# Performance work log

Hardware: AMD Instinct MI355X
Metric: run time of the kernel (lower is better)

Reference implementation:

```python
import jax, jax.numpy as jnp
import numpy as np

HID = 7168; H = 128; DQ = 1536; DKV = 512; DH = 128; DR = 64; MAXS = 4096

def _rope_tables(seq_len):
    inv_freq = 1.0 / (10000.0 ** (jnp.arange(0, DR, 2, dtype=jnp.float32) / DR))
    t = jnp.arange(seq_len, dtype=jnp.float32)
    freqs = jnp.outer(t, inv_freq)              # [S, DR/2]
    emb = jnp.concatenate([freqs, freqs], -1)   # [S, DR]
    return jnp.cos(emb), jnp.sin(emb)

def _apply_rope(x, cos, sin):
    # x: [..., S, DR]; cos/sin: [S, DR]
    d = x.shape[-1]
    x1, x2 = x[..., : d // 2], x[..., d // 2 :]
    rotated = jnp.concatenate([-x2, x1], -1)
    return (x * cos + rotated * sin).astype(x.dtype)

def setup_inputs() -> dict:
    key = jax.random.key(0)
    ks = jax.random.split(key, 16)
    s = 0.02
    inp = {
        "h":    jax.random.normal(ks[0], (1, 1024, HID), jnp.float32),
        "Wdq":  jax.random.normal(ks[1], (DQ, HID), jnp.float32) * s,
        "bdq":  jnp.zeros((DQ,), jnp.float32),
        "Wdkv": jax.random.normal(ks[2], (DKV, HID), jnp.float32) * s,
        "bdkv": jnp.zeros((DKV,), jnp.float32),
        "Wuq":  jax.random.normal(ks[3], (H * DH, DQ), jnp.float32) * s,
        "buq":  jnp.zeros((H * DH,), jnp.float32),
        "Wukv": jax.random.normal(ks[4], (H * DH * 2, DKV), jnp.float32) * s,
        "bukv": jnp.zeros((H * DH * 2,), jnp.float32),
        "Wrq":  jax.random.normal(ks[5], (H * DR, DQ), jnp.float32) * s,
        "brq":  jnp.zeros((H * DR,), jnp.float32),
        "Wrk":  jax.random.normal(ks[6], (DR, HID), jnp.float32) * s,
        "brk":  jnp.zeros((DR,), jnp.float32),
        "Wo":   jax.random.normal(ks[7], (HID, H * DH), jnp.float32) * s,
        "bo":   jnp.zeros((HID,), jnp.float32),
    }
    return inp

def reference(h, Wdq, bdq, Wdkv, bdkv, Wuq, buq, Wukv, bukv, Wrq, brq, Wrk, brk, Wo, bo):
    B, S, _ = h.shape
    c_q = h @ Wdq.T + bdq              # [B,S,DQ]
    c_kv = h @ Wdkv.T + bdkv           # [B,S,DKV]
    q_c = (c_q @ Wuq.T + buq).reshape(B, S, H, DH).transpose(0, 2, 1, 3)     # [B,H,S,DH]
    kv_c = (c_kv @ Wukv.T + bukv).reshape(B, S, H, 2 * DH).transpose(0, 2, 1, 3)
    k_c, v = kv_c[..., :DH], kv_c[..., DH:]                                  # [B,H,S,DH]
    q_r = (c_q @ Wrq.T + brq).reshape(B, S, H, DR).transpose(0, 2, 1, 3)     # [B,H,S,DR]
    k_r = (h @ Wrk.T + brk).reshape(B, S, 1, DR).transpose(0, 2, 1, 3)       # [B,1,S,DR]
    cos, sin = _rope_tables(S)
    q_r = _apply_rope(q_r, cos, sin)
    k_r = _apply_rope(k_r, cos, sin)
    q = jnp.concatenate([q_c, q_r], -1)                                      # [B,H,S,DH+DR]
    k = jnp.concatenate([k_c, jnp.broadcast_to(k_r, (B, H, S, DR))], -1)
    scale = 1.0 / jnp.sqrt(jnp.float32(DH + DR))
    scores = jnp.einsum('bhqd,bhkd->bhqk', q, k) * scale
    attn = jax.nn.softmax(scores, axis=-1)
    o = jnp.einsum('bhqk,bhkd->bhqd', attn, v)        # [B,H,S,DH]
    o = o.transpose(0, 2, 1, 3).reshape(B, S, H * DH)
    return o @ Wo.T + bo
```

## Files before the change

### kernel.cpp

```cpp
#include <hip/hip_runtime.h>
#include <hip/hip_bf16.h>

#define S_LEN 1024
#define HID 7168
#define NH 128
#define DQ 1536
#define DKV 512
#define DH 128
#define DR 64

typedef __attribute__((ext_vector_type(8))) short bf16x8;
typedef __attribute__((ext_vector_type(4))) float f32x4;
typedef __attribute__((ext_vector_type(4))) float fl4;
typedef __attribute__((ext_vector_type(4))) unsigned short us4;
typedef __attribute__((ext_vector_type(8))) unsigned short us8;
typedef __attribute__((ext_vector_type(4))) unsigned int u32x4;

static __device__ __forceinline__ unsigned short f2bf(float f) {
  union { float f; unsigned int u; } v; v.f = f;
  unsigned int u = v.u;
  return (unsigned short)((u + 0x7fffu + ((u >> 16) & 1u)) >> 16);
}
static __device__ __forceinline__ float bf2f(unsigned short u) {
  union { unsigned int u; float f; } v; v.u = ((unsigned int)u) << 16;
  return v.f;
}
static __device__ __forceinline__ unsigned int cvtpk2(float lo, float hi) {
  unsigned int r;
  asm("v_cvt_pk_bf16_f32 %0, %1, %2" : "=v"(r) : "v"(lo), "v"(hi));
  return r;
}

__global__ __launch_bounds__(256) void cvt_bf16_kernel(
    const float* __restrict__ in, unsigned short* __restrict__ out, int n8) {
  int i = blockIdx.x * 256 + threadIdx.x;
  int stride = gridDim.x * 256;
  for (; i < n8; i += stride) {
    fl4 a = ((const fl4*)in)[2 * i];
    fl4 b = ((const fl4*)in)[2 * i + 1];
    us8 u = { f2bf(a[0]), f2bf(a[1]), f2bf(a[2]), f2bf(a[3]),
              f2bf(b[0]), f2bf(b[1]), f2bf(b[2]), f2bf(b[3]) };
    ((us8*)out)[i] = u;
  }
}

template <int OUTMODE, int WFP32, int ROPEQ = 0>
__global__ __launch_bounds__(256) void gemm_k(
    const unsigned short* __restrict__ A, int lda,
    const unsigned short* __restrict__ Wb16,
    const float* __restrict__ Wfa, const float* __restrict__ Wfb, int nsplit,
    int ldw,
    const float* __restrict__ bias,
    void* __restrict__ Cv, int ldc, size_t zstride,
    int Ncl, int ksl, float alpha,
    const float* __restrict__ ctab = nullptr,
    const float* __restrict__ stab = nullptr)
{
  const int n0 = blockIdx.x * 128;
  if (n0 >= Ncl) return;

  __shared__ unsigned short As[128 * 64];
  __shared__ unsigned short Ws[128 * 64];
  const int t = threadIdx.x;
  const int l = t & 63, w = t >> 6;
  const int r15 = l & 15, g = l >> 4;
  const int wm = (w >> 1) * 64, wn = (w & 1) * 64;
  const int m0 = blockIdx.y * 128;
  const int kbase = blockIdx.z * ksl;
  const int srow = l >> 3;
  const int scol = (l & 7) * 8;

  f32x4 acc[4][4];
#pragma unroll
  for (int i = 0; i < 4; ++i)
#pragma unroll
    for (int j = 0; j < 4; ++j) acc[i][j] = (f32x4){0.f, 0.f, 0.f, 0.f};

  const unsigned short* Ab = A + (size_t)m0 * lda;
  const unsigned short* Wb = nullptr;
  const float* Wf = nullptr;
  if constexpr (WFP32) {
    Wf = (n0 < nsplit) ? Wfa + (size_t)n0 * ldw : Wfb + (size_t)(n0 - nsplit) * ldw;
  } else {
    Wb = Wb16 + (size_t)n0 * ldw;
  }

  fl4 wx[4], wy[4];
  auto issueW = [&](int k0) {
#pragma unroll
    for (int i = 0; i < 4; ++i) {
      int c = t + 256 * i;
      const float* src = Wf + (size_t)(c >> 3) * ldw + k0 + (c & 7) * 8;
      wx[i] = *(const fl4*)src;
      wy[i] = *(const fl4*)(src + 4);
    }
  };

  if constexpr (WFP32) issueW(kbase);
  const int kend = kbase + ksl;

  for (int k0 = kbase; k0 < kend; k0 += 64) {
    __syncthreads();
#pragma unroll
    for (int i = 0; i < 4; ++i) {
      int chunk = w * 4 + i;
      int row = chunk * 8 + srow;
      __builtin_amdgcn_global_load_lds(
          (const __attribute__((address_space(1))) void*)(Ab + (size_t)row * lda + k0 + scol),
          (__attribute__((address_space(3))) void*)(As + chunk * 512), 16, 0, 0);
      if constexpr (!WFP32) {
        __builtin_amdgcn_global_load_lds(
            (const __attribute__((address_space(1))) void*)(Wb + (size_t)row * ldw + k0 + scol),
            (__attribute__((address_space(3))) void*)(Ws + chunk * 512), 16, 0, 0);
      }
    }
    if constexpr (WFP32) {
#pragma unroll
      for (int i = 0; i < 4; ++i) {
        int c = t + 256 * i;
        u32x4 p = { cvtpk2(wx[i][0], wx[i][1]), cvtpk2(wx[i][2], wx[i][3]),
                    cvtpk2(wy[i][0], wy[i][1]), cvtpk2(wy[i][2], wy[i][3]) };
        ((u32x4*)Ws)[c] = p;
      }
    }
    __syncthreads();
    if constexpr (WFP32) {
      if (k0 + 64 < kend) issueW(k0 + 64);
    }
#pragma unroll
    for (int kk = 0; kk < 2; ++kk) {
      bf16x8 a[4], b[4];
#pragma unroll
      for (int mt = 0; mt < 4; ++mt)
        a[mt] = *reinterpret_cast<const bf16x8*>(&As[(wm + mt * 16 + r15) * 64 + kk * 32 + 8 * g]);
#pragma unroll
      for (int nt = 0; nt < 4; ++nt)
        b[nt] = *reinterpret_cast<const bf16x8*>(&Ws[(wn + nt * 16 + r15) * 64 + kk * 32 + 8 * g]);
#pragma unroll
      for (int mt = 0; mt < 4; ++mt)
#pragma unroll
        for (int nt = 0; nt < 4; ++nt)
          acc[mt][nt] = __builtin_amdgcn_mfma_f32_16x16x32_bf16(a[mt], b[nt], acc[mt][nt], 0, 0, 0);
    }
  }

  if constexpr (OUTMODE == 1) {
    float bv[4];
#pragma unroll
    for (int nt = 0; nt < 4; ++nt) {
      int col = n0 + wn + nt * 16 + r15;
      bv[nt] = (col < Ncl) ? bias[col] : 0.f;
    }
    bool isrope = false;
    if constexpr (ROPEQ) isrope = (n0 + wn) >= 16384;
    if (ROPEQ && isrope) {
#pragma unroll
      for (int mt = 0; mt < 4; ++mt)
#pragma unroll
        for (int r = 0; r < 4; ++r) {
          int row = m0 + wm + mt * 16 + g * 4 + r;
#pragma unroll
          for (int ntp = 0; ntp < 2; ++ntp) {
            int j = ntp * 16 + r15;
            float c = ctab[row * 32 + j];
            float s = stab[row * 32 + j];
            float x1 = acc[mt][ntp][r] + bv[ntp];
            float x2 = acc[mt][ntp + 2][r] + bv[ntp + 2];
            int col1 = n0 + wn + ntp * 16 + r15;
            ((unsigned short*)Cv)[(size_t)row * ldc + col1] =
                f2bf((x1 * c - x2 * s) * alpha);
            ((unsigned short*)Cv)[(size_t)row * ldc + col1 + 32] =
                f2bf((x2 * c + x1 * s) * alpha);
          }
        }
    } else {
#pragma unroll
      for (int mt = 0; mt < 4; ++mt)
#pragma unroll
        for (int nt = 0; nt < 4; ++nt) {
          int col = n0 + wn + nt * 16 + r15;
          if (col < Ncl) {
#pragma unroll
            for (int r = 0; r < 4; ++r) {
              int row = m0 + wm + mt * 16 + g * 4 + r;
              ((unsigned short*)Cv)[(size_t)row * ldc + col] =
                  f2bf((acc[mt][nt][r] + bv[nt]) * alpha);
            }
          }
        }
    }
  } else {
    float* Cp = (float*)Cv + blockIdx.z * zstride;
#pragma unroll
    for (int mt = 0; mt < 4; ++mt)
#pragma unroll
      for (int nt = 0; nt < 4; ++nt) {
        int col = n0 + wn + nt * 16 + r15;
        if (col < Ncl) {
#pragma unroll
          for (int r = 0; r < 4; ++r) {
            int row = m0 + wm + mt * 16 + g * 4 + r;
            Cp[(size_t)row * ldc + col] = acc[mt][nt][r];
          }
        }
      }
  }
}

__global__ __launch_bounds__(256) void gemm_g4(
    const unsigned short* __restrict__ A,
    const float* __restrict__ W,
    float* __restrict__ pbuf)
{
  __shared__ unsigned short As[128 * 64];
  __shared__ unsigned short Ws[128 * 64];
  const int t = threadIdx.x;
  const int l = t & 63, w = t >> 6;
  const int r15 = l & 15, g = l >> 4;
  const int wm = (w >> 1) * 64, wn = (w & 1) * 64;
  const int bid = blockIdx.x;
  const int z = bid / 448;
  const int r448 = bid % 448;
  const int grp = r448 >> 6, wi = r448 & 63;
  const int m0 = (wi >> 3) * 128;
  const int n0 = (grp * 8 + (wi & 7)) * 128;
  const int kbase = z * 4096;
  const int srow = l >> 3, scol = (l & 7) * 8;

  f32x4 acc[4][4];
#pragma unroll
  for (int i = 0; i < 4; ++i)
#pragma unroll
    for (int j = 0; j < 4; ++j) acc[i][j] = (f32x4){0.f, 0.f, 0.f, 0.f};

  const unsigned short* Ab = A + (size_t)m0 * 16384;
  const float* Wf = W + (size_t)n0 * 16384;

  fl4 wx[4], wy[4];
  auto issueW = [&](int k0) {
#pragma unroll
    for (int i = 0; i < 4; ++i) {
      int c = t + 256 * i;
      const float* src = Wf + (size_t)(c >> 3) * 16384 + k0 + (c & 7) * 8;
      wx[i] = *(const fl4*)src;
      wy[i] = *(const fl4*)(src + 4);
    }
  };
  issueW(kbase);
  const int kend = kbase + 4096;

  for (int k0 = kbase; k0 < kend; k0 += 64) {
    __syncthreads();
#pragma unroll
    for (int i = 0; i < 4; ++i) {
      int chunk = w * 4 + i;
      int row = chunk * 8 + srow;
      __builtin_amdgcn_global_load_lds(
          (const __attribute__((address_space(1))) void*)(Ab + (size_t)row * 16384 + k0 + scol),
          (__attribute__((address_space(3))) void*)(As + chunk * 512), 16, 0, 0);
    }
#pragma unroll
    for (int i = 0; i < 4; ++i) {
      int c = t + 256 * i;
      u32x4 p = { cvtpk2(wx[i][0], wx[i][1]), cvtpk2(wx[i][2], wx[i][3]),
                  cvtpk2(wy[i][0], wy[i][1]), cvtpk2(wy[i][2], wy[i][3]) };
      ((u32x4*)Ws)[c] = p;
    }
    __syncthreads();
    if (k0 + 64 < kend) issueW(k0 + 64);
#pragma unroll
    for (int kk = 0; kk < 2; ++kk) {
      bf16x8 a[4], b[4];
#pragma unroll
      for (int mt = 0; mt < 4; ++mt)
        a[mt] = *reinterpret_cast<const bf16x8*>(&As[(wm + mt * 16 + r15) * 64 + kk * 32 + 8 * g]);
#pragma unroll
      for (int nt = 0; nt < 4; ++nt)
        b[nt] = *reinterpret_cast<const bf16x8*>(&Ws[(wn + nt * 16 + r15) * 64 + kk * 32 + 8 * g]);
#pragma unroll
      for (int mt = 0; mt < 4; ++mt)
#pragma unroll
        for (int nt = 0; nt < 4; ++nt)
          acc[mt][nt] = __builtin_amdgcn_mfma_f32_16x16x32_bf16(a[mt], b[nt], acc[mt][nt], 0, 0, 0);
    }
  }

  float* Cp = pbuf + (size_t)z * 1024 * 7168;
#pragma unroll
  for (int mt = 0; mt < 4; ++mt)
#pragma unroll
    for (int nt = 0; nt < 4; ++nt) {
      int col = n0 + wn + nt * 16 + r15;
#pragma unroll
      for (int r = 0; r < 4; ++r) {
        int row = m0 + wm + mt * 16 + g * 4 + r;
        Cp[(size_t)row * 7168 + col] = acc[mt][nt][r];
      }
    }
}

__global__ __launch_bounds__(256) void reduce_f32_kernel(
    const float* __restrict__ pbuf, const float* __restrict__ bias,
    float* __restrict__ out, int ldo, int rowlen4, int nz, size_t zstride, int total4)
{
  int idx = blockIdx.x * 256 + threadIdx.x;
  if (idx >= total4) return;
  int r = idx / rowlen4, c4 = idx % rowlen4;
  fl4 acc = *(const fl4*)(bias + c4 * 4);
  for (int z = 0; z < nz; ++z)
    acc += *(const fl4*)(pbuf + z * zstride + (size_t)idx * 4);
  *(fl4*)(out + (size_t)r * ldo + c4 * 4) = acc;
}

__global__ __launch_bounds__(256) void reduce_bf16_kernel(
    const float* __restrict__ pbuf, const float* __restrict__ bias,
    unsigned short* __restrict__ out, int ldo, int rowlen4, int nz, size_t zstride, int total4)
{
  int idx = blockIdx.x * 256 + threadIdx.x;
  if (idx >= total4) return;
  int r = idx / rowlen4, c4 = idx % rowlen4;
  fl4 acc = *(const fl4*)(bias + c4 * 4);
  for (int z = 0; z < nz; ++z)
    acc += *(const fl4*)(pbuf + z * zstride + (size_t)idx * 4);
  us4 u = { f2bf(acc[0]), f2bf(acc[1]), f2bf(acc[2]), f2bf(acc[3]) };
  *(us4*)(out + (size_t)r * ldo + c4 * 4) = u;
}

__global__ __launch_bounds__(256) void rope_table_kernel(float* __restrict__ ctab,
                                                         float* __restrict__ stab) {
  int idx = blockIdx.x * 256 + threadIdx.x;
  if (idx >= S_LEN * 32) return;
  int j = idx & 31, s = idx >> 5;
  float invf = expf(-0.28782313662425574f * (float)j);
  float ang = (float)s * invf;
  ctab[idx] = cosf(ang);
  stab[idx] = sinf(ang);
}

__global__ void rope_bf16_kernel(unsigned short* __restrict__ x, int nh, int lda, int total,
                                 const float* __restrict__ ctab,
                                 const float* __restrict__ stab) {
  int idx = blockIdx.x * 256 + threadIdx.x;
  if (idx >= total) return;
  int j = idx & 31;
  int rest = idx >> 5;
  int hh = rest % nh;
  int s = rest / nh;
  float c = ctab[s * 32 + j], sn = stab[s * 32 + j];
  size_t base = (size_t)s * lda + hh * 64;
  float x1 = bf2f(x[base + j]), x2 = bf2f(x[base + j + 32]);
  x[base + j]      = f2bf(x1 * c - x2 * sn);
  x[base + j + 32] = f2bf(x2 * c + x1 * sn);
}

__global__ __launch_bounds__(256) void vtrans_kernel(
    const unsigned short* __restrict__ kvb, unsigned short* __restrict__ vt) {
  __shared__ unsigned short tl[64][72];
  const int s0 = blockIdx.x * 64;
  const int c0 = blockIdx.y * 64;
  const int t = threadIdx.x;
  const int rr = t >> 3, cc = (t & 7) * 8;
  const int hbase = (c0 >> 7) * 256 + 128 + (c0 & 127);
#pragma unroll
  for (int i = 0; i < 2; ++i) {
    int r = rr + i * 32;
    *reinterpret_cast<bf16x8*>(&tl[r][cc]) =
        *reinterpret_cast<const bf16x8*>(kvb + (size_t)(s0 + r) * 32768 + hbase + cc);
  }
  __syncthreads();
#pragma unroll
  for (int i = 0; i < 2; ++i) {
    int vc = rr + i * 32;
    unsigned short tmp[8];
#pragma unroll
    for (int j = 0; j < 8; ++j) tmp[j] = tl[cc + j][vc];
    *reinterpret_cast<bf16x8*>(&vt[(size_t)(c0 + vc) * 1024 + s0 + cc]) =
        *reinterpret_cast<bf16x8*>(tmp);
  }
}

__global__ __launch_bounds__(512) void mla_attn_kernel(
    const unsigned short* __restrict__ qcat,
    const unsigned short* __restrict__ kvb,
    const unsigned short* __restrict__ kr,
    const unsigned short* __restrict__ vt,
    unsigned short* __restrict__ obuf)
{
  __shared__ unsigned short Klds[64][200];
  __shared__ unsigned short Vlds[128][72];
  __shared__ unsigned short Plds[8][16][72];

  const int t = threadIdx.x;
  const int l = t & 63, w = t >> 6;
  const int r15 = l & 15, g = l >> 4;
  const int bid = blockIdx.x;
  const int orig = (bid & 7) * 128 + (bid >> 3);
  const int h = orig >> 3;
  const int q0 = (orig & 7) * 128;

  bf16x8 qf[6];
  const unsigned short* qrow = qcat + (size_t)(q0 + w * 16 + r15) * 24576;
#pragma unroll
  for (int kk = 0; kk < 4; ++kk)
    qf[kk] = *reinterpret_cast<const bf16x8*>(qrow + h * 128 + kk * 32 + 8 * g);
#pragma unroll
  for (int kk = 4; kk < 6; ++kk)
    qf[kk] = *reinterpret_cast<const bf16x8*>(qrow + 16384 + h * 64 + (kk - 4) * 32 + 8 * g);

  bf16x8 kreg[3], vreg[2];
  auto loadKV = [&](int kk0) {
#pragma unroll
    for (int i = 0; i < 3; ++i) {
      int c = t + 512 * i, row = c / 24, cb = c % 24;
      const unsigned short* src = (cb < 16)
          ? kvb + (size_t)(kk0 + row) * 32768 + h * 256 + cb * 8
          : kr + (size_t)(kk0 + row) * 2112 + (cb - 16) * 8;
      kreg[i] = *reinterpret_cast<const bf16x8*>(src);
    }
#pragma unroll
    for (int i = 0; i < 2; ++i) {
      int c = t + 512 * i, d = c >> 3, kb = c & 7;
      vreg[i] = *reinterpret_cast<const bf16x8*>(vt + ((size_t)h * 128 + d) * 1024 + kk0 + kb * 8);
    }
  };

  float m_r[4], l_r[4];
  f32x4 oacc[8];
#pragma unroll
  for (int r = 0; r < 4; ++r) { m_r[r] = -1e30f; l_r[r] = 0.f; }
#pragma unroll
  for (int d = 0; d < 8; ++d) oacc[d] = (f32x4){0.f, 0.f, 0.f, 0.f};

  loadKV(0);

  for (int kt = 0; kt < 16; ++kt) {
    __syncthreads();
#pragma unroll
    for (int i = 0; i < 3; ++i) {
      int c = t + 512 * i, row = c / 24, cb = c % 24;
      *reinterpret_cast<bf16x8*>(&Klds[row][cb * 8]) = kreg[i];
    }
#pragma unroll
    for (int i = 0; i < 2; ++i) {
      int c = t + 512 * i, d = c >> 3, kb = c & 7;
      *reinterpret_cast<bf16x8*>(&Vlds[d][kb * 8]) = vreg[i];
    }
    __syncthreads();
    if (kt < 15) loadKV((kt + 1) * 64);

    f32x4 sacc[4];
#pragma unroll
    for (int nt = 0; nt < 4; ++nt) sacc[nt] = (f32x4){0.f, 0.f, 0.f, 0.f};
    __builtin_amdgcn_s_setprio(1);
#pragma unroll
    for (int nt = 0; nt < 4; ++nt)
#pragma unroll
      for (int kk = 0; kk < 6; ++kk) {
        bf16x8 b = *reinterpret_cast<const bf16x8*>(&Klds[nt * 16 + r15][kk * 32 + 8 * g]);
        sacc[nt] = __builtin_amdgcn_mfma_f32_16x16x32_bf16(qf[kk], b, sacc[nt], 0, 0, 0);
      }
    __builtin_amdgcn_s_setprio(0);

    float sc[4], rsum[4];
#pragma unroll
    for (int r = 0; r < 4; ++r) {
      float mx = fmaxf(fmaxf(sacc[0][r], sacc[1][r]), fmaxf(sacc[2][r], sacc[3][r]));
      mx = fmaxf(mx, __shfl_xor(mx, 1));
      mx = fmaxf(mx, __shfl_xor(mx, 2));
      mx = fmaxf(mx, __shfl_xor(mx, 4));
      mx = fmaxf(mx, __shfl_xor(mx, 8));
      float mn = fmaxf(m_r[r], mx);
      sc[r] = __expf(m_r[r] - mn);
      m_r[r] = mn;
      rsum[r] = 0.f;
    }
#pragma unroll
    for (int nt = 0; nt < 4; ++nt)
#pragma unroll
      for (int r = 0; r < 4; ++r) {
        float p = __expf(sacc[nt][r] - m_r[r]);
        rsum[r] += p;
        Plds[w][g * 4 + r][nt * 16 + r15] = f2bf(p);
      }
#pragma unroll
    for (int r = 0; r < 4; ++r) {
      float s = rsum[r];
      s += __shfl_xor(s, 1);
      s += __shfl_xor(s, 2);
      s += __shfl_xor(s, 4);
      s += __shfl_xor(s, 8);
      l_r[r] = l_r[r] * sc[r] + s;
    }
#pragma unroll
    for (int d = 0; d < 8; ++d)
#pragma unroll
      for (int r = 0; r < 4; ++r) oacc[d][r] *= sc[r];

    bf16x8 pa0 = *reinterpret_cast<const bf16x8*>(&Plds[w][r15][8 * g]);
    bf16x8 pa1 = *reinterpret_cast<const bf16x8*>(&Plds[w][r15][32 + 8 * g]);
    __builtin_amdgcn_s_setprio(1);
#pragma unroll
    for (int dt = 0; dt < 8; ++dt) {
      bf16x8 v0 = *reinterpret_cast<const bf16x8*>(&Vlds[dt * 16 + r15][8 * g]);
      bf16x8 v1 = *reinterpret_cast<const bf16x8*>(&Vlds[dt * 16 + r15][32 + 8 * g]);
      oacc[dt] = __builtin_amdgcn_mfma_f32_16x16x32_bf16(pa0, v0, oacc[dt], 0, 0, 0);
      oacc[dt] = __builtin_amdgcn_mfma_f32_16x16x32_bf16(pa1, v1, oacc[dt], 0, 0, 0);
    }
    __builtin_amdgcn_s_setprio(0);
  }

#pragma unroll
  for (int dt = 0; dt < 8; ++dt)
#pragma unroll
    for (int r = 0; r < 4; ++r) {
      int row = q0 + w * 16 + g * 4 + r;
      int col = h * DH + dt * 16 + r15;
      obuf[(size_t)row * 16384 + col] = f2bf(oacc[dt][r] / l_r[r]);
    }
}

extern "C" void kernel_launch(void* const* d_in, const int* in_sizes, int n_in,
                              void* d_out, int out_size, void* d_ws, size_t ws_size,
                              hipStream_t stream) {
  const float* h    = (const float*)d_in[0];
  const float* Wdq  = (const float*)d_in[1];
  const float* bdq  = (const float*)d_in[2];
  const float* Wdkv = (const float*)d_in[3];
  const float* bdkv = (const float*)d_in[4];
  const float* Wuq  = (const float*)d_in[5];
  const float* buq  = (const float*)d_in[6];
  const float* Wukv = (const float*)d_in[7];
  const float* bukv = (const float*)d_in[8];
  const float* Wrq  = (const float*)d_in[9];
  const float* brq  = (const float*)d_in[10];
  const float* Wrk  = (const float*)d_in[11];
  const float* brk  = (const float*)d_in[12];
  const float* Wo   = (const float*)d_in[13];
  const float* bo   = (const float*)d_in[14];
  float* out = (float*)d_out;

  char* ws = (char*)d_ws;
  size_t off = 0;
  auto alloc = [&](size_t bytes) {
    char* p = ws + off;
    off += (bytes + 255) & ~(size_t)255;
    return p;
  };
  unsigned short* hb    = (unsigned short*)alloc((size_t)1024 * 7168 * 2);
  unsigned short* W1cat = (unsigned short*)alloc((size_t)2176 * 7168 * 2);
  float*          b1cat = (float*)alloc(2176 * 4);
  unsigned short* ccat  = (unsigned short*)alloc((size_t)1024 * 2112 * 2);
  float*          b2cat = (float*)alloc(24576 * 4);
  unsigned short* qcat  = (unsigned short*)alloc((size_t)1024 * 24576 * 2);
  unsigned short* kvbb  = (unsigned short*)alloc((size_t)1024 * 32768 * 2);
  unsigned short* vt    = (unsigned short*)alloc((size_t)16384 * 1024 * 2);
  unsigned short* obuf  = (unsigned short*)alloc((size_t)1024 * 16384 * 2);
  float*          ctab  = (float*)alloc((size_t)S_LEN * 32 * 4);
  float*          stab  = (float*)alloc((size_t)S_LEN * 32 * 4);
  float* pbufG1 = (float*)qcat;
  float* pbufG4 = (float*)(ws + ((size_t)544 << 20));

  auto cvt = [&](const float* in, unsigned short* outp, size_t n) {
    int n8 = (int)(n / 8);
    int blocks = (n8 + 255) / 256;
    if (blocks > 2048) blocks = 2048;
    cvt_bf16_kernel<<<blocks, 256, 0, stream>>>(in, outp, n8);
  };

  cvt(h,    hb,    (size_t)1024 * 7168);
  cvt(Wdq,  W1cat, (size_t)1536 * 7168);
  cvt(Wdkv, W1cat + (size_t)1536 * 7168, (size_t)512 * 7168);
  cvt(Wrk,  W1cat + (size_t)2048 * 7168, (size_t)64 * 7168);
  hipMemsetAsync(W1cat + (size_t)2112 * 7168, 0, (size_t)64 * 7168 * 2, stream);
  hipMemcpyAsync(b1cat,        bdq,  1536 * 4, hipMemcpyDeviceToDevice, stream);
  hipMemcpyAsync(b1cat + 1536, bdkv, 512 * 4,  hipMemcpyDeviceToDevice, stream);
  hipMemcpyAsync(b1cat + 2048, brk,  64 * 4,   hipMemcpyDeviceToDevice, stream);
  hipMemsetAsync(b1cat + 2112, 0, 64 * 4, stream);
  hipMemcpyAsync(b2cat,         buq, 16384 * 4, hipMemcpyDeviceToDevice, stream);
  hipMemcpyAsync(b2cat + 16384, brq, 8192 * 4,  hipMemcpyDeviceToDevice, stream);
  rope_table_kernel<<<(S_LEN * 32 + 255) / 256, 256, 0, stream>>>(ctab, stab);

  const float scale = 0.07216878364870323f;
  const int BIGN = 1 << 30;
  dim3 blk(256);

  gemm_k<2, 0><<<dim3(24, 8, 4), blk, 0, stream>>>(
      hb, 7168, W1cat, nullptr, nullptr, BIGN, 7168, nullptr,
      pbufG1, 2112, (size_t)1024 * 2112, 2112, 1792, 1.0f);
  reduce_bf16_kernel<<<2112, blk, 0, stream>>>(pbufG1, b1cat, ccat, 2112, 528, 4,
                                               (size_t)1024 * 2112, 1024 * 2112 / 4);
  rope_bf16_kernel<<<(1024 * 32 + 255) / 256, blk, 0, stream>>>(ccat + 2048, 1, 2112, 1024 * 32, ctab, stab);

  gemm_k<1, 1, 1><<<dim3(192, 8, 1), blk, 0, stream>>>(
      ccat, 2112, nullptr, Wuq, Wrq, 16384, 1536, b2cat,
      qcat, 24576, 0, 24576, 1536, scale, ctab, stab);

  gemm_k<1, 1><<<dim3(256, 8, 1), blk, 0, stream>>>(
      ccat + 1536, 2112, nullptr, Wukv, Wukv, BIGN, 512, bukv,
      kvbb, 32768, 0, 32768, 512, 1.0f);
  vtrans_kernel<<<dim3(16, 256), blk, 0, stream>>>(kvbb, vt);
  mla_attn_kernel<<<dim3(1024), dim3(512), 0, stream>>>(qcat, kvbb, ccat + 2048, vt, obuf);

  gemm_g4<<<dim3(1792), blk, 0, stream>>>(obuf, Wo, pbufG4);
  reduce_f32_kernel<<<7168, blk, 0, stream>>>(pbufG4, bo, out,
                                              7168, 1792, 4, (size_t)1024 * 7168, 1024 * 7168 / 4);
}
```

Baseline: 1.124 ms.

## Replace syncthreads with manual waitcnt barriers and halve split-K in output GEMM

In the fp32-weight GEMM paths, full __syncthreads is replaced by raw s_barrier plus explicit partial vmcnt waits, so the next tile's weight prefetch stays in flight across the barrier instead of being drained. The output projection GEMM moves from 4-way to 2-way split-K (896 blocks, 8192 K each), and the reduce kernel sums 2 partials instead of 4. This cuts partial-sum traffic and reduce work but halves the grid, which may lower occupancy and load balance. The hand-written waitcnt counts must match the actual load ordering or the kernel will read stale data.

```diff
diff --git a/kernel.cpp b/kernel.cpp
--- a/kernel.cpp
+++ b/kernel.cpp
@@ -100,7 +100,12 @@
   const int kend = kbase + ksl;
 
   for (int k0 = kbase; k0 < kend; k0 += 64) {
-    __syncthreads();
+    if constexpr (WFP32) {
+      __builtin_amdgcn_s_barrier();
+      __builtin_amdgcn_sched_barrier(0);
+    } else {
+      __syncthreads();
+    }
 #pragma unroll
     for (int i = 0; i < 4; ++i) {
       int chunk = w * 4 + i;
@@ -115,6 +120,9 @@
       }
     }
     if constexpr (WFP32) {
+      __builtin_amdgcn_sched_barrier(0);
+      asm volatile("s_waitcnt vmcnt(4)" ::: "memory");
+      __builtin_amdgcn_sched_barrier(0);
 #pragma unroll
       for (int i = 0; i < 4; ++i) {
         int c = t + 256 * i;
@@ -122,10 +130,17 @@
                     cvtpk2(wy[i][0], wy[i][1]), cvtpk2(wy[i][2], wy[i][3]) };
         ((u32x4*)Ws)[c] = p;
       }
-    }
-    __syncthreads();
-    if constexpr (WFP32) {
-      if (k0 + 64 < kend) issueW(k0 + 64);
+      if (k0 + 64 < kend) {
+        issueW(k0 + 64);
+        __builtin_amdgcn_sched_barrier(0);
+        asm volatile("s_waitcnt vmcnt(8) lgkmcnt(0)" ::: "memory");
+      } else {
+        asm volatile("s_waitcnt vmcnt(0) lgkmcnt(0)" ::: "memory");
+      }
+      __builtin_amdgcn_sched_barrier(0);
+      __builtin_amdgcn_s_barrier();
+    } else {
+      __syncthreads();
     }
 #pragma unroll
     for (int kk = 0; kk < 2; ++kk) {
@@ -224,7 +239,7 @@
   const int grp = r448 >> 6, wi = r448 & 63;
   const int m0 = (wi >> 3) * 128;
   const int n0 = (grp * 8 + (wi & 7)) * 128;
-  const int kbase = z * 4096;
+  const int kbase = z * 8192;
   const int srow = l >> 3, scol = (l & 7) * 8;
 
   f32x4 acc[4][4];
@@ -247,10 +262,11 @@
     }
   };
   issueW(kbase);
-  const int kend = kbase + 4096;
+  const int kend = kbase + 8192;
 
   for (int k0 = kbase; k0 < kend; k0 += 64) {
-    __syncthreads();
+    __builtin_amdgcn_s_barrier();
+    __builtin_amdgcn_sched_barrier(0);
 #pragma unroll
     for (int i = 0; i < 4; ++i) {
       int chunk = w * 4 + i;
@@ -259,6 +275,9 @@
           (const __attribute__((address_space(1))) void*)(Ab + (size_t)row * 16384 + k0 + scol),
           (__attribute__((address_space(3))) void*)(As + chunk * 512), 16, 0, 0);
     }
+    __builtin_amdgcn_sched_barrier(0);
+    asm volatile("s_waitcnt vmcnt(4)" ::: "memory");
+    __builtin_amdgcn_sched_barrier(0);
 #pragma unroll
     for (int i = 0; i < 4; ++i) {
       int c = t + 256 * i;
@@ -266,8 +285,15 @@
                   cvtpk2(wy[i][0], wy[i][1]), cvtpk2(wy[i][2], wy[i][3]) };
       ((u32x4*)Ws)[c] = p;
     }
-    __syncthreads();
-    if (k0 + 64 < kend) issueW(k0 + 64);
+    if (k0 + 64 < kend) {
+      issueW(k0 + 64);
+      __builtin_amdgcn_sched_barrier(0);
+      asm volatile("s_waitcnt vmcnt(8) lgkmcnt(0)" ::: "memory");
+    } else {
+      asm volatile("s_waitcnt vmcnt(0) lgkmcnt(0)" ::: "memory");
+    }
+    __builtin_amdgcn_sched_barrier(0);
+    __builtin_amdgcn_s_barrier();
 #pragma unroll
     for (int kk = 0; kk < 2; ++kk) {
       bf16x8 a[4], b[4];
@@ -549,8 +575,8 @@
   unsigned short* hb    = (unsigned short*)alloc((size_t)1024 * 7168 * 2);
   unsigned short* W1cat = (unsigned short*)alloc((size_t)2176 * 7168 * 2);
   float*          b1cat = (float*)alloc(2176 * 4);
+  float*          b2cat = (float*)alloc(24576 * 4);
   unsigned short* ccat  = (unsigned short*)alloc((size_t)1024 * 2112 * 2);
-  float*          b2cat = (float*)alloc(24576 * 4);
   unsigned short* qcat  = (unsigned short*)alloc((size_t)1024 * 24576 * 2);
   unsigned short* kvbb  = (unsigned short*)alloc((size_t)1024 * 32768 * 2);
   unsigned short* vt    = (unsigned short*)alloc((size_t)16384 * 1024 * 2);
@@ -601,7 +627,7 @@
   vtrans_kernel<<<dim3(16, 256), blk, 0, stream>>>(kvbb, vt);
   mla_attn_kernel<<<dim3(1024), dim3(512), 0, stream>>>(qcat, kvbb, ccat + 2048, vt, obuf);
 
-  gemm_g4<<<dim3(1792), blk, 0, stream>>>(obuf, Wo, pbufG4);
+  gemm_g4<<<dim3(896), blk, 0, stream>>>(obuf, Wo, pbufG4);
   reduce_f32_kernel<<<7168, blk, 0, stream>>>(pbufG4, bo, out,
-                                              7168, 1792, 4, (size_t)1024 * 7168, 1024 * 7168 / 4);
-}
+                                              7168, 1792, 2, (size_t)1024 * 7168, 1024 * 7168 / 4);
+}
```

Result: no change. 1.122 ms (-0.2%).
